# Optimization experiments

Hardware: AMD Instinct MI355X
Metric: run time of the kernel (lower is better)

## Reference

```python
import jax, jax.numpy as jnp
import numpy as np

EPS = 1e-20
SCALE = 1.0 / np.sqrt(128.0).astype(np.float32)


def setup_inputs() -> dict:
    key = jax.random.key(0)
    k1, k2 = jax.random.split(key)
    B, K, J, I = 64, 16, 512, 128
    inputs = jax.random.normal(k1, (B, J, I), dtype=jnp.float32)
    W = jax.random.normal(k2, (K, J, I), dtype=jnp.float32)
    b = jnp.zeros((K, J, 1), dtype=jnp.float32)
    return {"inputs": inputs, "W": W, "b": b}


def _squash(s):
    # squash(v) = (1 - 1/(exp(||v||)+eps)) * v / (||v|| + eps), norm over last dim
    n = jnp.linalg.norm(s, axis=-1, keepdims=True)
    return (1.0 - 1.0 / (jnp.exp(n) + EPS)) * (s / (n + EPS))


def reference(inputs, W, b):
    # inputs: (B, J, I); W: (K, J, I); b: (K, J, 1)
    u = inputs[..., None, :, :] * W            # (B, K, J, I) broadcast multiply
    c = jnp.sum(u * u, axis=-1, keepdims=True) * SCALE  # (B, K, J, 1)
    c = jax.nn.softmax(c, axis=0)              # softmax over BATCH dim, as in source
    c = c + b                                  # bias broadcast over batch
    s = jnp.sum(u * c, axis=-2)                # (B, K, I) weighted sum over in_channel
    return _squash(s)
```

## Files before the change

kernel.cpp:

```cpp
#include <hip/hip_runtime.h>
#include <math.h>

#define B 64
#define K 16
#define J 512
#define I 128
#define SCALE 0.08838834764831845f
#define EPSF 1e-20f
#define JC 32
#define JCW 16

typedef __attribute__((ext_vector_type(8))) short short8;
typedef __attribute__((ext_vector_type(4))) float f32x4;
typedef __attribute__((ext_vector_type(2))) float f32x2;

static __device__ __forceinline__ unsigned f2bf(float f) {
    union { float f; unsigned u; } v; v.f = f;
    return (v.u + 0x7FFFu + ((v.u >> 16) & 1u)) >> 16;
}

__global__ __launch_bounds__(256) void k1_mfma(const float* __restrict__ x,
                                               const float* __restrict__ w,
                                               const float* __restrict__ bias,
                                               float* __restrict__ cw2) {
    __shared__ __align__(16) char lds[80 * 256];
    char* lx = lds;
    char* lw = lds + 64 * 256;

    const int raw = blockIdx.x;
    const int j = (raw & 7) * 64 + (raw >> 3);
    const int tid = threadIdx.x;

#pragma unroll
    for (int r = 0; r < 8; ++r) {
        int item = tid + 256 * r;
        int row = item >> 5, q = item & 31;
        float4 v = *(const float4*)(x + ((size_t)row * J + j) * I + q * 4);
        uint2 u;
        u.x = f2bf(v.x * v.x) | (f2bf(v.y * v.y) << 16);
        u.y = f2bf(v.z * v.z) | (f2bf(v.w * v.w) << 16);
        *(uint2*)(lx + row * 256 + ((q * 8) ^ ((row & 7) << 4))) = u;
    }
#pragma unroll
    for (int r = 0; r < 2; ++r) {
        int item = tid + 256 * r;
        int k = item >> 5, q = item & 31;
        float4 v = *(const float4*)(w + ((size_t)k * J + j) * I + q * 4);
        uint2 u;
        u.x = f2bf(v.x * v.x) | (f2bf(v.y * v.y) << 16);
        u.y = f2bf(v.z * v.z) | (f2bf(v.w * v.w) << 16);
        *(uint2*)(lw + k * 256 + ((q * 8) ^ ((k & 7) << 4))) = u;
    }
    __syncthreads();
    if (tid >= 64) return;

    const int g = tid >> 4, n = tid & 15;
    f32x4 acc[4];
#pragma unroll
    for (int t = 0; t < 4; ++t) acc[t] = (f32x4){0.f, 0.f, 0.f, 0.f};

#pragma unroll
    for (int s = 0; s < 4; ++s) {
        const int colb = s * 64 + g * 16;
        short8 af = *(const short8*)(lw + n * 256 + (colb ^ ((n & 7) << 4)));
#pragma unroll
        for (int t = 0; t < 4; ++t) {
            int row = t * 16 + n;
            short8 bf = *(const short8*)(lx + row * 256 + (colb ^ ((row & 7) << 4)));
            acc[t] = __builtin_amdgcn_mfma_f32_16x16x32_bf16(af, bf, acc[t], 0, 0, 0);
        }
    }

#pragma unroll
    for (int r = 0; r < 4; ++r) {
        float s0 = acc[0][r] * SCALE, s1 = acc[1][r] * SCALE;
        float s2 = acc[2][r] * SCALE, s3 = acc[3][r] * SCALE;
        float mx = fmaxf(fmaxf(s0, s1), fmaxf(s2, s3));
#pragma unroll
        for (int msk = 1; msk <= 8; msk <<= 1) mx = fmaxf(mx, __shfl_xor(mx, msk, 64));
        float e0 = expf(s0 - mx), e1 = expf(s1 - mx);
        float e2 = expf(s2 - mx), e3 = expf(s3 - mx);
        float sum = e0 + e1 + e2 + e3;
#pragma unroll
        for (int msk = 1; msk <= 8; msk <<= 1) sum += __shfl_xor(sum, msk, 64);
        float inv = 1.f / sum;
        float bi = bias[(g * 4 + r) * J + j];
        size_t base = (((size_t)g * 8) * 512 + j) * 32 + r * 8 + (n & 7);
        size_t btoff = (size_t)(n >> 3) * 512 * 32;
        cw2[base + btoff + (size_t)0 * 2 * 512 * 32] = e0 * inv + bi;
        cw2[base + btoff + (size_t)1 * 2 * 512 * 32] = e1 * inv + bi;
        cw2[base + btoff + (size_t)2 * 2 * 512 * 32] = e2 * inv + bi;
        cw2[base + btoff + (size_t)3 * 2 * 512 * 32] = e3 * inv + bi;
    }
}

__global__ __launch_bounds__(256) void k3_wsum(const float* __restrict__ x,
                                               const float* __restrict__ w,
                                               const float* __restrict__ cw2,
                                               float* __restrict__ sp) {
    __shared__ float cl[JCW * 32];
    __shared__ __align__(16) float2 red[4][16][64];

    const int raw = blockIdx.x;
    const int swz = (raw & 7) * 128 + (raw >> 3);
    const int kt = swz & 3, bt = (swz >> 2) & 7, jh = swz >> 5;
    const int j0 = jh * JCW, b0 = bt * 8, k0 = kt * 4;

    const int lane = threadIdx.x & 63;
    const int wvi  = threadIdx.x >> 6;

    if (threadIdx.x < 128)
        ((float4*)cl)[threadIdx.x] =
            ((const float4*)(cw2 + ((size_t)(kt * 8 + bt) * 512 + j0) * 32))[threadIdx.x];
    __syncthreads();

    float2 acc[8][4];
#pragma unroll
    for (int bb = 0; bb < 8; ++bb)
#pragma unroll
        for (int kk = 0; kk < 4; ++kk) acc[bb][kk] = make_float2(0.f, 0.f);

#pragma unroll
    for (int it = 0; it < 4; ++it) {
        const int j = j0 + wvi * 4 + it;
        float2 xv[8], wv[4];
#pragma unroll
        for (int bb = 0; bb < 8; ++bb)
            xv[bb] = *(const float2*)(x + ((size_t)(b0 + bb) * J + j) * I + lane * 2);
#pragma unroll
        for (int kk = 0; kk < 4; ++kk)
            wv[kk] = *(const float2*)(w + ((size_t)(k0 + kk) * J + j) * I + lane * 2);
        const float* cj = cl + (j - j0) * 32;
#pragma unroll
        for (int kk = 0; kk < 4; ++kk) {
            float4 cA = *(const float4*)(cj + kk * 8);
            float4 cB = *(const float4*)(cj + kk * 8 + 4);
            acc[0][kk].x = fmaf(xv[0].x * wv[kk].x, cA.x, acc[0][kk].x);
            acc[0][kk].y = fmaf(xv[0].y * wv[kk].y, cA.x, acc[0][kk].y);
            acc[1][kk].x = fmaf(xv[1].x * wv[kk].x, cA.y, acc[1][kk].x);
            acc[1][kk].y = fmaf(xv[1].y * wv[kk].y, cA.y, acc[1][kk].y);
            acc[2][kk].x = fmaf(xv[2].x * wv[kk].x, cA.z, acc[2][kk].x);
            acc[2][kk].y = fmaf(xv[2].y * wv[kk].y, cA.z, acc[2][kk].y);
            acc[3][kk].x = fmaf(xv[3].x * wv[kk].x, cA.w, acc[3][kk].x);
            acc[3][kk].y = fmaf(xv[3].y * wv[kk].y, cA.w, acc[3][kk].y);
            acc[4][kk].x = fmaf(xv[4].x * wv[kk].x, cB.x, acc[4][kk].x);
            acc[4][kk].y = fmaf(xv[4].y * wv[kk].y, cB.x, acc[4][kk].y);
            acc[5][kk].x = fmaf(xv[5].x * wv[kk].x, cB.y, acc[5][kk].x);
            acc[5][kk].y = fmaf(xv[5].y * wv[kk].y, cB.y, acc[5][kk].y);
            acc[6][kk].x = fmaf(xv[6].x * wv[kk].x, cB.z, acc[6][kk].x);
            acc[6][kk].y = fmaf(xv[6].y * wv[kk].y, cB.z, acc[6][kk].y);
            acc[7][kk].x = fmaf(xv[7].x * wv[kk].x, cB.w, acc[7][kk].x);
            acc[7][kk].y = fmaf(xv[7].y * wv[kk].y, cB.w, acc[7][kk].y);
        }
    }

#pragma unroll
    for (int bbl = 0; bbl < 4; ++bbl)
#pragma unroll
        for (int kk = 0; kk < 4; ++kk)
            red[wvi][bbl * 4 + kk][lane] = acc[bbl][kk];
    __syncthreads();
#pragma unroll
    for (int s = 0; s < 4; ++s) {
        int slot = wvi + 4 * s;
        float2 a = red[0][slot][lane];
        float2 b = red[1][slot][lane];
        float2 c = red[2][slot][lane];
        float2 d = red[3][slot][lane];
        f32x2 v = {a.x + b.x + c.x + d.x, a.y + b.y + c.y + d.y};
        int bb = slot >> 2, kk = slot & 3;
        __builtin_nontemporal_store(
            v, (f32x2*)(sp + (((size_t)jh * B + b0 + bb) * K + k0 + kk) * I + lane * 2));
    }
    __syncthreads();
#pragma unroll
    for (int bbl = 0; bbl < 4; ++bbl)
#pragma unroll
        for (int kk = 0; kk < 4; ++kk)
            red[wvi][bbl * 4 + kk][lane] = acc[4 + bbl][kk];
    __syncthreads();
#pragma unroll
    for (int s = 0; s < 4; ++s) {
        int slot = wvi + 4 * s;
        float2 a = red[0][slot][lane];
        float2 b = red[1][slot][lane];
        float2 c = red[2][slot][lane];
        float2 d = red[3][slot][lane];
        f32x2 v = {a.x + b.x + c.x + d.x, a.y + b.y + c.y + d.y};
        int bb = (slot >> 2) + 4, kk = slot & 3;
        __builtin_nontemporal_store(
            v, (f32x2*)(sp + (((size_t)jh * B + b0 + bb) * K + k0 + kk) * I + lane * 2));
    }
}

__global__ __launch_bounds__(256) void k4_squash(const float* __restrict__ sp,
                                                 float* __restrict__ out) {
    const int wv = threadIdx.x >> 6;
    const int lane = threadIdx.x & 63;
    const int bk = blockIdx.x * 4 + wv;
    const int b = bk >> 4, k = bk & 15;

    float s0 = 0.f, s1 = 0.f;
#pragma unroll
    for (int p = 0; p < JC; ++p) {
        f32x2 v = __builtin_nontemporal_load(
            (const f32x2*)(sp + (((size_t)p * B + b) * K + k) * I + lane * 2));
        s0 += v.x; s1 += v.y;
    }
    float q = s0 * s0 + s1 * s1;
#pragma unroll
    for (int m = 32; m >= 1; m >>= 1) q += __shfl_xor(q, m, 64);

    float n = sqrtf(q);
    float factor = (1.0f - 1.0f / (expf(n) + EPSF)) / (n + EPSF);
    f32x2 o = {s0 * factor, s1 * factor};
    __builtin_nontemporal_store(
        o, (f32x2*)(out + ((size_t)b * K + k) * I + lane * 2));
}

extern "C" void kernel_launch(void* const* d_in, const int* in_sizes, int n_in,
                              void* d_out, int out_size, void* d_ws, size_t ws_size,
                              hipStream_t stream) {
    const float* x    = (const float*)d_in[0];
    const float* w    = (const float*)d_in[1];
    const float* bias = (const float*)d_in[2];
    float* out = (float*)d_out;

    float* cw2 = (float*)d_ws;
    float* sp  = cw2 + (size_t)K * J * B;

    hipLaunchKernelGGL(k1_mfma,  dim3(512),  dim3(256), 0, stream, x, w, bias, cw2);
    hipLaunchKernelGGL(k3_wsum,  dim3(1024), dim3(256), 0, stream, x, w, cw2, sp);
    hipLaunchKernelGGL(k4_squash, dim3(256), dim3(256), 0, stream, sp, out);
}
```

Before: 24.83 us.

## Stage fp16 copies of x and W in a chunk-local layout for the weighted sum

The first kernel now writes fp16 copies of inputs and weights, laid out by j-chunk, while it reads them for the routing logits. The weighted-sum kernel reads these half-size copies instead of the fp32 originals, halving its global load bytes and improving locality per block. In exchange the first kernel does extra global writes, and the weighted sum loses precision by rounding x and W to fp16.

```diff
diff --git a/kernel.cpp b/kernel.cpp
--- a/kernel.cpp
+++ b/kernel.cpp
@@ -13,6 +13,8 @@
 typedef __attribute__((ext_vector_type(8))) short short8;
 typedef __attribute__((ext_vector_type(4))) float f32x4;
 typedef __attribute__((ext_vector_type(2))) float f32x2;
+typedef __attribute__((ext_vector_type(2))) _Float16 f16x2;
+typedef __attribute__((ext_vector_type(4))) _Float16 f16x4;
 
 static __device__ __forceinline__ unsigned f2bf(float f) {
     union { float f; unsigned u; } v; v.f = f;
@@ -22,13 +24,17 @@
 __global__ __launch_bounds__(256) void k1_mfma(const float* __restrict__ x,
                                                const float* __restrict__ w,
                                                const float* __restrict__ bias,
-                                               float* __restrict__ cw2) {
+                                               float* __restrict__ cw2,
+                                               _Float16* __restrict__ xh,
+                                               _Float16* __restrict__ wh) {
     __shared__ __align__(16) char lds[80 * 256];
     char* lx = lds;
     char* lw = lds + 64 * 256;
 
     const int raw = blockIdx.x;
     const int j = (raw & 7) * 64 + (raw >> 3);
+    const int jc2 = raw & 7;
+    const int jl = raw >> 3;
     const int tid = threadIdx.x;
 
 #pragma unroll
@@ -36,6 +42,8 @@
         int item = tid + 256 * r;
         int row = item >> 5, q = item & 31;
         float4 v = *(const float4*)(x + ((size_t)row * J + j) * I + q * 4);
+        f16x4 h = {(_Float16)v.x, (_Float16)v.y, (_Float16)v.z, (_Float16)v.w};
+        *(f16x4*)(xh + (((size_t)jc2 * B + row) * 64 + jl) * I + q * 4) = h;
         uint2 u;
         u.x = f2bf(v.x * v.x) | (f2bf(v.y * v.y) << 16);
         u.y = f2bf(v.z * v.z) | (f2bf(v.w * v.w) << 16);
@@ -46,6 +54,8 @@
         int item = tid + 256 * r;
         int k = item >> 5, q = item & 31;
         float4 v = *(const float4*)(w + ((size_t)k * J + j) * I + q * 4);
+        f16x4 h = {(_Float16)v.x, (_Float16)v.y, (_Float16)v.z, (_Float16)v.w};
+        *(f16x4*)(wh + (((size_t)jc2 * K + k) * 64 + jl) * I + q * 4) = h;
         uint2 u;
         u.x = f2bf(v.x * v.x) | (f2bf(v.y * v.y) << 16);
         u.y = f2bf(v.z * v.z) | (f2bf(v.w * v.w) << 16);
@@ -94,8 +104,8 @@
     }
 }
 
-__global__ __launch_bounds__(256) void k3_wsum(const float* __restrict__ x,
-                                               const float* __restrict__ w,
+__global__ __launch_bounds__(256) void k3_wsum(const _Float16* __restrict__ xh,
+                                               const _Float16* __restrict__ wh,
                                                const float* __restrict__ cw2,
                                                float* __restrict__ sp) {
     __shared__ float cl[JCW * 32];
@@ -105,6 +115,8 @@
     const int swz = (raw & 7) * 128 + (raw >> 3);
     const int kt = swz & 3, bt = (swz >> 2) & 7, jh = swz >> 5;
     const int j0 = jh * JCW, b0 = bt * 8, k0 = kt * 4;
+    const int jc2 = jh >> 2;
+    const int jlb = (jh & 3) * JCW;
 
     const int lane = threadIdx.x & 63;
     const int wvi  = threadIdx.x >> 6;
@@ -122,15 +134,20 @@
 
 #pragma unroll
     for (int it = 0; it < 4; ++it) {
-        const int j = j0 + wvi * 4 + it;
+        const int jli = wvi * 4 + it;
+        const int jl = jlb + jli;
         float2 xv[8], wv[4];
 #pragma unroll
-        for (int bb = 0; bb < 8; ++bb)
-            xv[bb] = *(const float2*)(x + ((size_t)(b0 + bb) * J + j) * I + lane * 2);
-#pragma unroll
-        for (int kk = 0; kk < 4; ++kk)
-            wv[kk] = *(const float2*)(w + ((size_t)(k0 + kk) * J + j) * I + lane * 2);
-        const float* cj = cl + (j - j0) * 32;
+        for (int bb = 0; bb < 8; ++bb) {
+            f16x2 h = *(const f16x2*)(xh + (((size_t)jc2 * B + b0 + bb) * 64 + jl) * I + lane * 2);
+            xv[bb] = make_float2((float)h.x, (float)h.y);
+        }
+#pragma unroll
+        for (int kk = 0; kk < 4; ++kk) {
+            f16x2 h = *(const f16x2*)(wh + (((size_t)jc2 * K + k0 + kk) * 64 + jl) * I + lane * 2);
+            wv[kk] = make_float2((float)h.x, (float)h.y);
+        }
+        const float* cj = cl + jli * 32;
 #pragma unroll
         for (int kk = 0; kk < 4; ++kk) {
             float4 cA = *(const float4*)(cj + kk * 8);
@@ -228,8 +245,12 @@
 
     float* cw2 = (float*)d_ws;
     float* sp  = cw2 + (size_t)K * J * B;
-
-    hipLaunchKernelGGL(k1_mfma,  dim3(512),  dim3(256), 0, stream, x, w, bias, cw2);
-    hipLaunchKernelGGL(k3_wsum,  dim3(1024), dim3(256), 0, stream, x, w, cw2, sp);
+    _Float16* xh = (_Float16*)(sp + (size_t)JC * B * K * I);
+    _Float16* wh = xh + (size_t)B * J * I;
+
+    hipLaunchKernelGGL(k1_mfma,  dim3(512),  dim3(256), 0, stream,
+                       x, w, bias, cw2, xh, wh);
+    hipLaunchKernelGGL(k3_wsum,  dim3(1024), dim3(256), 0, stream,
+                       xh, wh, cw2, sp);
     hipLaunchKernelGGL(k4_squash, dim3(256), dim3(256), 0, stream, sp, out);
 }
```

New measurement: 24.69 us. No clear change (-0.6%).

## Split k3 waves over batch instead of j to drop shared-memory reduction

Applied to the files above, without the earlier changes.

Each wave in the weighted-sum kernel now owns two batch rows and walks all 16 j values, instead of owning 4 j values for all 8 batches. Every wave holds complete partial sums, so the LDS reduction buffer and its barriers go away and each wave stores its results directly. In exchange, each wave now reloads the same W rows, so W traffic through the caches rises fourfold, and each wave carries a longer serial chain of loads per j.

```diff
diff --git a/kernel.cpp b/kernel.cpp
--- a/kernel.cpp
+++ b/kernel.cpp
@@ -99,7 +99,6 @@
                                                const float* __restrict__ cw2,
                                                float* __restrict__ sp) {
     __shared__ float cl[JCW * 32];
-    __shared__ __align__(16) float2 red[4][16][64];
 
     const int raw = blockIdx.x;
     const int swz = (raw & 7) * 128 + (raw >> 3);
@@ -114,83 +113,44 @@
             ((const float4*)(cw2 + ((size_t)(kt * 8 + bt) * 512 + j0) * 32))[threadIdx.x];
     __syncthreads();
 
-    float2 acc[8][4];
+    const int b = b0 + 2 * wvi;
+    const float* xp0 = x + ((size_t)b * J + j0) * I + lane * 2;
+    const float* xp1 = xp0 + (size_t)J * I;
+    const float* wp  = w + ((size_t)k0 * J + j0) * I + lane * 2;
+
+    float2 acc[2][4];
 #pragma unroll
-    for (int bb = 0; bb < 8; ++bb)
+    for (int bb = 0; bb < 2; ++bb)
 #pragma unroll
         for (int kk = 0; kk < 4; ++kk) acc[bb][kk] = make_float2(0.f, 0.f);
 
 #pragma unroll
-    for (int it = 0; it < 4; ++it) {
-        const int j = j0 + wvi * 4 + it;
-        float2 xv[8], wv[4];
-#pragma unroll
-        for (int bb = 0; bb < 8; ++bb)
-            xv[bb] = *(const float2*)(x + ((size_t)(b0 + bb) * J + j) * I + lane * 2);
+    for (int jl = 0; jl < JCW; ++jl) {
+        float2 x0 = *(const float2*)(xp0 + jl * I);
+        float2 x1 = *(const float2*)(xp1 + jl * I);
+        float2 wv[4];
 #pragma unroll
         for (int kk = 0; kk < 4; ++kk)
-            wv[kk] = *(const float2*)(w + ((size_t)(k0 + kk) * J + j) * I + lane * 2);
-        const float* cj = cl + (j - j0) * 32;
+            wv[kk] = *(const float2*)(wp + ((size_t)kk * J + jl) * I);
+        const float* cj = cl + jl * 32 + 2 * wvi;
 #pragma unroll
         for (int kk = 0; kk < 4; ++kk) {
-            float4 cA = *(const float4*)(cj + kk * 8);
-            float4 cB = *(const float4*)(cj + kk * 8 + 4);
-            acc[0][kk].x = fmaf(xv[0].x * wv[kk].x, cA.x, acc[0][kk].x);
-            acc[0][kk].y = fmaf(xv[0].y * wv[kk].y, cA.x, acc[0][kk].y);
-            acc[1][kk].x = fmaf(xv[1].x * wv[kk].x, cA.y, acc[1][kk].x);
-            acc[1][kk].y = fmaf(xv[1].y * wv[kk].y, cA.y, acc[1][kk].y);
-            acc[2][kk].x = fmaf(xv[2].x * wv[kk].x, cA.z, acc[2][kk].x);
-            acc[2][kk].y = fmaf(xv[2].y * wv[kk].y, cA.z, acc[2][kk].y);
-            acc[3][kk].x = fmaf(xv[3].x * wv[kk].x, cA.w, acc[3][kk].x);
-            acc[3][kk].y = fmaf(xv[3].y * wv[kk].y, cA.w, acc[3][kk].y);
-            acc[4][kk].x = fmaf(xv[4].x * wv[kk].x, cB.x, acc[4][kk].x);
-            acc[4][kk].y = fmaf(xv[4].y * wv[kk].y, cB.x, acc[4][kk].y);
-            acc[5][kk].x = fmaf(xv[5].x * wv[kk].x, cB.y, acc[5][kk].x);
-            acc[5][kk].y = fmaf(xv[5].y * wv[kk].y, cB.y, acc[5][kk].y);
-            acc[6][kk].x = fmaf(xv[6].x * wv[kk].x, cB.z, acc[6][kk].x);
-            acc[6][kk].y = fmaf(xv[6].y * wv[kk].y, cB.z, acc[6][kk].y);
-            acc[7][kk].x = fmaf(xv[7].x * wv[kk].x, cB.w, acc[7][kk].x);
-            acc[7][kk].y = fmaf(xv[7].y * wv[kk].y, cB.w, acc[7][kk].y);
+            float2 cc = *(const float2*)(cj + kk * 8);
+            acc[0][kk].x = fmaf(x0.x * wv[kk].x, cc.x, acc[0][kk].x);
+            acc[0][kk].y = fmaf(x0.y * wv[kk].y, cc.x, acc[0][kk].y);
+            acc[1][kk].x = fmaf(x1.x * wv[kk].x, cc.y, acc[1][kk].x);
+            acc[1][kk].y = fmaf(x1.y * wv[kk].y, cc.y, acc[1][kk].y);
         }
     }
 
 #pragma unroll
-    for (int bbl = 0; bbl < 4; ++bbl)
+    for (int bb = 0; bb < 2; ++bb)
 #pragma unroll
-        for (int kk = 0; kk < 4; ++kk)
-            red[wvi][bbl * 4 + kk][lane] = acc[bbl][kk];
-    __syncthreads();
-#pragma unroll
-    for (int s = 0; s < 4; ++s) {
-        int slot = wvi + 4 * s;
-        float2 a = red[0][slot][lane];
-        float2 b = red[1][slot][lane];
-        float2 c = red[2][slot][lane];
-        float2 d = red[3][slot][lane];
-        f32x2 v = {a.x + b.x + c.x + d.x, a.y + b.y + c.y + d.y};
-        int bb = slot >> 2, kk = slot & 3;
-        __builtin_nontemporal_store(
-            v, (f32x2*)(sp + (((size_t)jh * B + b0 + bb) * K + k0 + kk) * I + lane * 2));
-    }
-    __syncthreads();
-#pragma unroll
-    for (int bbl = 0; bbl < 4; ++bbl)
-#pragma unroll
-        for (int kk = 0; kk < 4; ++kk)
-            red[wvi][bbl * 4 + kk][lane] = acc[4 + bbl][kk];
-    __syncthreads();
-#pragma unroll
-    for (int s = 0; s < 4; ++s) {
-        int slot = wvi + 4 * s;
-        float2 a = red[0][slot][lane];
-        float2 b = red[1][slot][lane];
-        float2 c = red[2][slot][lane];
-        float2 d = red[3][slot][lane];
-        f32x2 v = {a.x + b.x + c.x + d.x, a.y + b.y + c.y + d.y};
-        int bb = (slot >> 2) + 4, kk = slot & 3;
-        __builtin_nontemporal_store(
-            v, (f32x2*)(sp + (((size_t)jh * B + b0 + bb) * K + k0 + kk) * I + lane * 2));
-    }
+        for (int kk = 0; kk < 4; ++kk) {
+            f32x2 v = {acc[bb][kk].x, acc[bb][kk].y};
+            __builtin_nontemporal_store(
+                v, (f32x2*)(sp + (((size_t)jh * B + b + bb) * K + k0 + kk) * I + lane * 2));
+        }
 }
 
 __global__ __launch_bounds__(256) void k4_squash(const float* __restrict__ sp,
```

Result: slower. 28.68 us (+15.5%).
